# Performance work log

Hardware: AMD Instinct MI355X
Metric: run time of the kernel (lower is better)

## Reference

```python
import jax, jax.numpy as jnp
import numpy as np

K = 9          # kernel_size
PAD = K // 2   # same padding
SIGMA = 1.0
EPS = 1e-5     # BatchNorm eps


def setup_inputs() -> dict:
    key = jax.random.key(0)
    k0, k1, k2 = jax.random.split(key, 3)
    B, Cin, Cout, L = 4, 64, 64, 131072
    x = jax.random.normal(k0, (B, Cin, L), jnp.float32)
    coords = jax.random.uniform(k1, (B, 3, L), jnp.float32)  # 3D point coords in [0,1)
    W = jax.random.normal(k2, (Cout, Cin, K), jnp.float32) * (1.0 / np.sqrt(Cin * K))
    bias = jnp.zeros((Cout,), jnp.float32)
    gamma = jnp.ones((Cout,), jnp.float32)
    beta = jnp.zeros((Cout,), jnp.float32)
    return {"x": x, "coords": coords, "W": W, "bias": bias, "gamma": gamma, "beta": beta}


def reference(x, coords, W, bias, gamma, beta):
    B, Cin, L = x.shape
    # zero-pad sequence dim for 'same' conv
    xpad = jnp.pad(x, ((0, 0), (0, 0), (PAD, PAD)))
    cpad = jnp.pad(coords, ((0, 0), (0, 0), (PAD, PAD)))
    # unfold: neighbor windows of size K (K is a small compile-time constant)
    x_unf = jnp.stack([xpad[:, :, k:k + L] for k in range(K)], axis=2)   # [B,Cin,K,L]
    c_unf = jnp.stack([cpad[:, :, k:k + L] for k in range(K)], axis=2)   # [B,3,K,L]
    # Gaussian spatial weights from coord distances (WeightedConv1D)
    dist2 = jnp.sum((c_unf - coords[:, :, None, :]) ** 2, axis=1)        # [B,K,L]
    w = jnp.exp(-dist2 / (2.0 * SIGMA * SIGMA))                          # [B,K,L]
    # weighted conv: contract over (Cin, K)
    out = jnp.einsum('ock,bckl->bol', W, x_unf * w[:, None, :, :])       # [B,Cout,L]
    out = out + bias[None, :, None]
    # BatchNorm1d (training-mode batch statistics over B and L) + ReLU
    mean = out.mean(axis=(0, 2), keepdims=True)
    var = out.var(axis=(0, 2), keepdims=True)
    out = (out - mean) * jax.lax.rsqrt(var + EPS)
    out = out * gamma[None, :, None] + beta[None, :, None]
    return jax.nn.relu(out)
```

## Files before the change

kernel.cpp:

```cpp
#include <hip/hip_runtime.h>
#include <hip/hip_bf16.h>

#define KK 9
#define PADK 4
#define CIN 64
#define COUT 64
#define LSEQ 131072
#define NB 4
#define TILEL 128
#define XROWS 136
#define XRS 72
#define NTILES 1024
#define NPART 64

typedef __attribute__((ext_vector_type(8))) short v8s;
typedef __attribute__((ext_vector_type(4))) float v4f;

__device__ __forceinline__ unsigned short f2bf(float f) {
  __hip_bfloat16 h = __float2bfloat16(f);
  return *reinterpret_cast<unsigned short*>(&h);
}
__device__ __forceinline__ float bf2f(unsigned short s) {
  return __uint_as_float(((unsigned)s) << 16);
}

__device__ __forceinline__ void store_o(float* p, float v) { *p = v; }
__device__ __forceinline__ void store_o(__hip_bfloat16* p, float v) { *p = __float2bfloat16(v); }

template <int CTRL>
__device__ __forceinline__ float dppadd(float v) {
  int s = __builtin_amdgcn_update_dpp(0, __float_as_int(v), CTRL, 0xF, 0xF, true);
  return v + __int_as_float(s);
}
__device__ __forceinline__ float red16(float v) {
  v = dppadd<0xB1>(v);
  v = dppadd<0x4E>(v);
  v = dppadd<0x141>(v);
  v = dppadd<0x140>(v);
  return v;
}

__global__ void wtrans_kernel(const float* __restrict__ W, v8s* __restrict__ Wt) {
  int t = blockIdx.x * 256 + threadIdx.x;
  if (t >= KK * 2 * 4 * 64) return;
  int lane = t & 63;
  int frag = t >> 6;
  int mblk = frag & 3;
  int s    = (frag >> 2) & 1;
  int k    = frag >> 3;
  int m = lane & 15, q = lane >> 4;
  int o = mblk * 16 + m;
  union { v8s v; unsigned short h[8]; } u;
#pragma unroll
  for (int j = 0; j < 8; ++j) {
    int c = 32 * s + q * 8 + j;
    u.h[j] = f2bf(W[(o * CIN + c) * KK + k]);
  }
  Wt[t] = u.v;
}

template <typename OutT>
__global__ __launch_bounds__(256, 5)
void conv_kernel(const float* __restrict__ x, const float* __restrict__ coords,
                 const v8s* __restrict__ Wt, OutT* __restrict__ cv,
                 float* __restrict__ stat_sum, float* __restrict__ stat_sq) {
  __shared__ __align__(16) __hip_bfloat16 xt[XROWS][XRS];
  __shared__ float wt[KK][TILEL];

  const int tid  = threadIdx.x;
  const int wv   = tid >> 6;
  const int wo   = wv & 1;
  const int wl   = wv >> 1;
  const int lane = tid & 63;
  const int gw   = blockIdx.x;
  const int b    = gw >> 10;
  const int tile = gw & (NTILES - 1);
  const int l0   = tile * TILEL;
  const float* xb = x + (b * CIN) * LSEQ;
  const float* cb = coords + (b * 3) * LSEQ;
  const int m = lane & 15;
  const int q = lane >> 4;

  {
    int cg = tid & 7;
    int lc = tid >> 3;
    int c8 = cg * 8;
    float4 f[8];
#pragma unroll
    for (int t = 0; t < 8; ++t)
      f[t] = *(const float4*)(xb + (c8 + t) * LSEQ + l0 + 4 * lc);
    const float* fp = (const float*)&f[0];
#pragma unroll
    for (int j = 0; j < 4; ++j) {
      union { v8s v; unsigned short h[8]; } u;
#pragma unroll
      for (int t = 0; t < 8; ++t) u.h[t] = f2bf(fp[4 * t + j]);
      *(v8s*)&xt[4 + 4 * lc + j][c8] = u.v;
    }
  }
  if (tid < 128) {
    int side = tid >> 6;
    int c = tid & 63;
    if (side == 0) {
      float el[4] = {0.f, 0.f, 0.f, 0.f};
      if (tile != 0) {
#pragma unroll
        for (int j = 0; j < 4; ++j) el[j] = xb[c * LSEQ + l0 - 4 + j];
      }
#pragma unroll
      for (int j = 0; j < 4; ++j) xt[j][c] = __float2bfloat16(el[j]);
    } else {
      float er[4] = {0.f, 0.f, 0.f, 0.f};
      if (tile != NTILES - 1) {
#pragma unroll
        for (int j = 0; j < 4; ++j) er[j] = xb[c * LSEQ + l0 + TILEL + j];
      }
#pragma unroll
      for (int j = 0; j < 4; ++j) xt[128 + 4 + j][c] = __float2bfloat16(er[j]);
    }
  }
  if (tid < TILEL) {
    int n = tid;
    float sx = cb[l0 + n];
    float sy = cb[LSEQ + l0 + n];
    float sz = cb[2 * LSEQ + l0 + n];
#pragma unroll
    for (int k = 0; k < KK; ++k) {
      int l = l0 + n + k - PADK;
      float cx = 0.f, cy = 0.f, cz = 0.f;
      if ((unsigned)l < (unsigned)LSEQ) {
        cx = cb[l]; cy = cb[LSEQ + l]; cz = cb[2 * LSEQ + l];
      }
      float dx = cx - sx, dy = cy - sy, dz = cz - sz;
      wt[k][n] = __expf(-0.5f * (dx * dx + dy * dy + dz * dz));
    }
  }
  __syncthreads();

  v4f tot[2][4];
#pragma unroll
  for (int i = 0; i < 2; ++i)
#pragma unroll
    for (int j = 0; j < 4; ++j)
      tot[i][j] = (v4f){0.f, 0.f, 0.f, 0.f};

  const v4f z4 = (v4f){0.f, 0.f, 0.f, 0.f};
  const v8s* wp = Wt + (wo * 2) * 64 + lane;

#pragma unroll 1
  for (int k = 0; k < KK; ++k) {
    v8s a00 = wp[k * 512];
    v8s a10 = wp[k * 512 + 64];
    v8s a01 = wp[k * 512 + 256];
    v8s a11 = wp[k * 512 + 256 + 64];
#pragma unroll
    for (int nbq = 0; nbq < 4; ++nbq) {
      const __hip_bfloat16* xr = &xt[wl * 64 + nbq * 16 + m + k][0];
      v8s bf0 = *(const v8s*)(xr + q * 8);
      v8s bf1 = *(const v8s*)(xr + q * 8 + 32);
      float wk = wt[k][wl * 64 + nbq * 16 + m];
      v4f y0 = __builtin_amdgcn_mfma_f32_16x16x32_bf16(a00, bf0, z4, 0, 0, 0);
      y0     = __builtin_amdgcn_mfma_f32_16x16x32_bf16(a01, bf1, y0, 0, 0, 0);
      v4f y1 = __builtin_amdgcn_mfma_f32_16x16x32_bf16(a10, bf0, z4, 0, 0, 0);
      y1     = __builtin_amdgcn_mfma_f32_16x16x32_bf16(a11, bf1, y1, 0, 0, 0);
#pragma unroll
      for (int r = 0; r < 4; ++r) {
        tot[0][nbq][r] = __builtin_fmaf(wk, y0[r], tot[0][nbq][r]);
        tot[1][nbq][r] = __builtin_fmaf(wk, y1[r], tot[1][nbq][r]);
      }
    }
  }

  const int part = gw & (NPART - 1);
  OutT* outb = cv + (size_t)(b * COUT) * LSEQ;
#pragma unroll
  for (int mb = 0; mb < 2; ++mb) {
#pragma unroll
    for (int r = 0; r < 4; ++r) {
      int o = wo * 32 + mb * 16 + q * 4 + r;
      float s1 = 0.f, s2 = 0.f;
#pragma unroll
      for (int nbq = 0; nbq < 4; ++nbq) {
        float v = tot[mb][nbq][r];
        s1 += v;
        s2 += v * v;
        store_o(&outb[o * LSEQ + l0 + wl * 64 + nbq * 16 + m], v);
      }
      s1 = red16(s1);
      s2 = red16(s2);
      if (m == 0) {
        atomicAdd(&stat_sum[part * COUT + o], s1);
        atomicAdd(&stat_sq [part * COUT + o], s2);
      }
    }
  }
}

__global__ __launch_bounds__(256)
void finalize_kernel(const float* __restrict__ stat_sum,
                     const float* __restrict__ stat_sq,
                     const float* __restrict__ gamma,
                     const float* __restrict__ beta,
                     float* __restrict__ ss) {
  __shared__ float red[2][4][COUT];
  const int o = threadIdx.x & 63, pq = threadIdx.x >> 6;
  float s1 = 0.f, s2 = 0.f;
#pragma unroll 4
  for (int p = pq * 16; p < pq * 16 + 16; ++p) {
    s1 += stat_sum[p * COUT + o];
    s2 += stat_sq [p * COUT + o];
  }
  red[0][pq][o] = s1;
  red[1][pq][o] = s2;
  __syncthreads();
  if (threadIdx.x < 64) {
    float t1 = red[0][0][o] + red[0][1][o] + red[0][2][o] + red[0][3][o];
    float t2 = red[1][0][o] + red[1][1][o] + red[1][2][o] + red[1][3][o];
    const float invN = 1.0f / (float)(NB * LSEQ);
    float mean = t1 * invN;
    float var  = t2 * invN - mean * mean;
    float sc = gamma[o] * rsqrtf(var + 1e-5f);
    ss[o]        = sc;
    ss[COUT + o] = beta[o] - mean * sc;
  }
}

__global__ __launch_bounds__(256)
void scale_f32_kernel(float* __restrict__ data, const float* __restrict__ ss) {
  const int blk = blockIdx.x;
  const int ch = (blk >> 6) & 63;
  const float sc = ss[ch];
  const float sh = ss[COUT + ch];
  const int base = blk * 2048 + threadIdx.x * 8;
  float4 a = *(float4*)(data + base);
  float4 b = *(float4*)(data + base + 4);
  a.x = fmaxf(fmaf(a.x, sc, sh), 0.f);
  a.y = fmaxf(fmaf(a.y, sc, sh), 0.f);
  a.z = fmaxf(fmaf(a.z, sc, sh), 0.f);
  a.w = fmaxf(fmaf(a.w, sc, sh), 0.f);
  b.x = fmaxf(fmaf(b.x, sc, sh), 0.f);
  b.y = fmaxf(fmaf(b.y, sc, sh), 0.f);
  b.z = fmaxf(fmaf(b.z, sc, sh), 0.f);
  b.w = fmaxf(fmaf(b.w, sc, sh), 0.f);
  *(float4*)(data + base)     = a;
  *(float4*)(data + base + 4) = b;
}

__global__ __launch_bounds__(256)
void scale_bf16_kernel(const __hip_bfloat16* __restrict__ cvin,
                       const float* __restrict__ ss, float* __restrict__ out) {
  const int blk = blockIdx.x;
  const int ch = (blk >> 6) & 63;
  const float sc = ss[ch];
  const float sh = ss[COUT + ch];
  const int base = blk * 2048 + threadIdx.x * 8;
  union { v8s v; unsigned short h[8]; } u;
  u.v = *(const v8s*)(cvin + base);
  float r[8];
#pragma unroll
  for (int i = 0; i < 8; ++i)
    r[i] = fmaxf(fmaf(bf2f(u.h[i]), sc, sh), 0.f);
  *(float4*)(out + base)     = make_float4(r[0], r[1], r[2], r[3]);
  *(float4*)(out + base + 4) = make_float4(r[4], r[5], r[6], r[7]);
}

extern "C" void kernel_launch(void* const* d_in, const int* in_sizes, int n_in,
                              void* d_out, int out_size, void* d_ws, size_t ws_size,
                              hipStream_t stream) {
  const float* x      = (const float*)d_in[0];
  const float* coords = (const float*)d_in[1];
  const float* W      = (const float*)d_in[2];
  const float* gamma  = (const float*)d_in[4];
  const float* beta   = (const float*)d_in[5];
  float* out = (float*)d_out;
  char* ws = (char*)d_ws;

  float* stat_sum = (float*)(ws);
  float* stat_sq  = (float*)(ws + 16384);
  float* ss       = (float*)(ws + 32768);
  v8s*   Wt       = (v8s*)(ws + 40960);
  __hip_bfloat16* scratch = (__hip_bfloat16*)(ws + 131072);

  const size_t need_bf16 = (size_t)131072 + (size_t)NB * COUT * LSEQ * 2;
  const bool bf16_path = ws_size >= need_bf16;

  hipMemsetAsync(ws, 0, 32768, stream);
  wtrans_kernel<<<18, 256, 0, stream>>>(W, Wt);

  if (bf16_path) {
    conv_kernel<__hip_bfloat16><<<NB * NTILES, 256, 0, stream>>>(
        x, coords, Wt, scratch, stat_sum, stat_sq);
    finalize_kernel<<<1, 256, 0, stream>>>(stat_sum, stat_sq, gamma, beta, ss);
    scale_bf16_kernel<<<(NB * COUT * (LSEQ / 2048)), 256, 0, stream>>>(scratch, ss, out);
  } else {
    conv_kernel<float><<<NB * NTILES, 256, 0, stream>>>(
        x, coords, Wt, out, stat_sum, stat_sq);
    finalize_kernel<<<1, 256, 0, stream>>>(stat_sum, stat_sq, gamma, beta, ss);
    scale_f32_kernel<<<(NB * COUT * (LSEQ / 2048)), 256, 0, stream>>>(out, ss);
  }
}
```

Measured before the change: 320.5 us.

## Process two tiles per block with register prefetch of next tile

Each conv block now handles two consecutive sequence tiles, halving the grid. While the MFMA loop runs on the current tile, the x, halo and coord values for the next tile are loaded into registers. The Gaussian weight computation is split across all 256 threads instead of 128. This aims to hide global load latency behind compute, at the cost of more registers (possibly lower occupancy under launch_bounds 5) and fewer blocks to spread across the GPU.

```diff
diff --git a/kernel.cpp b/kernel.cpp
--- a/kernel.cpp
+++ b/kernel.cpp
@@ -12,6 +12,8 @@
 #define XRS 72
 #define NTILES 1024
 #define NPART 64
+#define TPB 2
+#define GRIDC (NB * NTILES / TPB)
 
 typedef __attribute__((ext_vector_type(8))) short v8s;
 typedef __attribute__((ext_vector_type(4))) float v4f;
@@ -72,125 +74,147 @@
   const int wo   = wv & 1;
   const int wl   = wv >> 1;
   const int lane = tid & 63;
-  const int gw   = blockIdx.x;
-  const int b    = gw >> 10;
-  const int tile = gw & (NTILES - 1);
-  const int l0   = tile * TILEL;
+  const int m = lane & 15;
+  const int q = lane >> 4;
+
+  const int bid = blockIdx.x;
+  const int b   = bid >> 9;
+  const int t0  = (bid & 511) * TPB;
   const float* xb = x + (b * CIN) * LSEQ;
   const float* cb = coords + (b * 3) * LSEQ;
-  const int m = lane & 15;
-  const int q = lane >> 4;
-
-  {
-    int cg = tid & 7;
-    int lc = tid >> 3;
-    int c8 = cg * 8;
-    float4 f[8];
+  OutT* outb = cv + (size_t)(b * COUT) * LSEQ;
+
+  const int cg8 = tid & 7, lc = tid >> 3, c8 = cg8 * 8;
+  const int cn = tid & 127, kh = tid >> 7, k0 = kh * 4;
+  const int nk = kh ? 5 : 4;
+
+  float4 f[8];
+  float4 hx;
+  float sx, sy, sz;
+  float nx[5], ny[5], nz[5];
+
+  auto prefetch = [&](int tile) {
+    const int l0 = tile * TILEL;
 #pragma unroll
     for (int t = 0; t < 8; ++t)
       f[t] = *(const float4*)(xb + (c8 + t) * LSEQ + l0 + 4 * lc);
-    const float* fp = (const float*)&f[0];
-#pragma unroll
-    for (int j = 0; j < 4; ++j) {
-      union { v8s v; unsigned short h[8]; } u;
-#pragma unroll
-      for (int t = 0; t < 8; ++t) u.h[t] = f2bf(fp[4 * t + j]);
-      *(v8s*)&xt[4 + 4 * lc + j][c8] = u.v;
-    }
-  }
-  if (tid < 128) {
-    int side = tid >> 6;
-    int c = tid & 63;
-    if (side == 0) {
-      float el[4] = {0.f, 0.f, 0.f, 0.f};
-      if (tile != 0) {
-#pragma unroll
-        for (int j = 0; j < 4; ++j) el[j] = xb[c * LSEQ + l0 - 4 + j];
-      }
-#pragma unroll
-      for (int j = 0; j < 4; ++j) xt[j][c] = __float2bfloat16(el[j]);
-    } else {
-      float er[4] = {0.f, 0.f, 0.f, 0.f};
-      if (tile != NTILES - 1) {
-#pragma unroll
-        for (int j = 0; j < 4; ++j) er[j] = xb[c * LSEQ + l0 + TILEL + j];
-      }
-#pragma unroll
-      for (int j = 0; j < 4; ++j) xt[128 + 4 + j][c] = __float2bfloat16(er[j]);
-    }
-  }
-  if (tid < TILEL) {
-    int n = tid;
-    float sx = cb[l0 + n];
-    float sy = cb[LSEQ + l0 + n];
-    float sz = cb[2 * LSEQ + l0 + n];
-#pragma unroll
+    if (tid < 128) {
+      int side = tid >> 6, c = tid & 63;
+      hx = make_float4(0.f, 0.f, 0.f, 0.f);
+      if (side == 0) {
+        if (tile != 0) hx = *(const float4*)(xb + c * LSEQ + l0 - 4);
+      } else {
+        if (tile != NTILES - 1) hx = *(const float4*)(xb + c * LSEQ + l0 + TILEL);
+      }
+    }
+    sx = cb[l0 + cn];
+    sy = cb[LSEQ + l0 + cn];
+    sz = cb[2 * LSEQ + l0 + cn];
+#pragma unroll
+    for (int i = 0; i < 5; ++i) {
+      int l = l0 + cn + (k0 + i) - PADK;
+      float cx = 0.f, cy = 0.f, cz = 0.f;
+      if (i < nk && (unsigned)l < (unsigned)LSEQ) {
+        cx = cb[l]; cy = cb[LSEQ + l]; cz = cb[2 * LSEQ + l];
+      }
+      nx[i] = cx; ny[i] = cy; nz[i] = cz;
+    }
+  };
+
+  prefetch(t0);
+
+#pragma unroll 1
+  for (int ti = 0; ti < TPB; ++ti) {
+    const int tile = t0 + ti;
+    const int l0 = tile * TILEL;
+
+    {
+      const float* fp = (const float*)&f[0];
+#pragma unroll
+      for (int j = 0; j < 4; ++j) {
+        union { v8s v; unsigned short h[8]; } u;
+#pragma unroll
+        for (int t = 0; t < 8; ++t) u.h[t] = f2bf(fp[4 * t + j]);
+        *(v8s*)&xt[4 + 4 * lc + j][c8] = u.v;
+      }
+      if (tid < 128) {
+        int side = tid >> 6, c = tid & 63;
+        int rb = side ? (TILEL + PADK) : 0;
+        xt[rb + 0][c] = __float2bfloat16(hx.x);
+        xt[rb + 1][c] = __float2bfloat16(hx.y);
+        xt[rb + 2][c] = __float2bfloat16(hx.z);
+        xt[rb + 3][c] = __float2bfloat16(hx.w);
+      }
+#pragma unroll
+      for (int i = 0; i < 5; ++i) {
+        if (i < nk) {
+          float dx = nx[i] - sx, dy = ny[i] - sy, dz = nz[i] - sz;
+          wt[k0 + i][cn] = __expf(-0.5f * (dx * dx + dy * dy + dz * dz));
+        }
+      }
+    }
+
+    if (ti + 1 < TPB) prefetch(tile + 1);
+
+    asm volatile("s_waitcnt lgkmcnt(0)" ::: "memory");
+    __builtin_amdgcn_s_barrier();
+
+    v4f tot[2][4];
+#pragma unroll
+    for (int i = 0; i < 2; ++i)
+#pragma unroll
+      for (int j = 0; j < 4; ++j)
+        tot[i][j] = (v4f){0.f, 0.f, 0.f, 0.f};
+
+    const v4f z4 = (v4f){0.f, 0.f, 0.f, 0.f};
+    const v8s* wp = Wt + (wo * 2) * 64 + lane;
+
+#pragma unroll 1
     for (int k = 0; k < KK; ++k) {
-      int l = l0 + n + k - PADK;
-      float cx = 0.f, cy = 0.f, cz = 0.f;
-      if ((unsigned)l < (unsigned)LSEQ) {
-        cx = cb[l]; cy = cb[LSEQ + l]; cz = cb[2 * LSEQ + l];
-      }
-      float dx = cx - sx, dy = cy - sy, dz = cz - sz;
-      wt[k][n] = __expf(-0.5f * (dx * dx + dy * dy + dz * dz));
-    }
-  }
-  __syncthreads();
-
-  v4f tot[2][4];
-#pragma unroll
-  for (int i = 0; i < 2; ++i)
-#pragma unroll
-    for (int j = 0; j < 4; ++j)
-      tot[i][j] = (v4f){0.f, 0.f, 0.f, 0.f};
-
-  const v4f z4 = (v4f){0.f, 0.f, 0.f, 0.f};
-  const v8s* wp = Wt + (wo * 2) * 64 + lane;
-
-#pragma unroll 1
-  for (int k = 0; k < KK; ++k) {
-    v8s a00 = wp[k * 512];
-    v8s a10 = wp[k * 512 + 64];
-    v8s a01 = wp[k * 512 + 256];
-    v8s a11 = wp[k * 512 + 256 + 64];
-#pragma unroll
-    for (int nbq = 0; nbq < 4; ++nbq) {
-      const __hip_bfloat16* xr = &xt[wl * 64 + nbq * 16 + m + k][0];
-      v8s bf0 = *(const v8s*)(xr + q * 8);
-      v8s bf1 = *(const v8s*)(xr + q * 8 + 32);
-      float wk = wt[k][wl * 64 + nbq * 16 + m];
-      v4f y0 = __builtin_amdgcn_mfma_f32_16x16x32_bf16(a00, bf0, z4, 0, 0, 0);
-      y0     = __builtin_amdgcn_mfma_f32_16x16x32_bf16(a01, bf1, y0, 0, 0, 0);
-      v4f y1 = __builtin_amdgcn_mfma_f32_16x16x32_bf16(a10, bf0, z4, 0, 0, 0);
-      y1     = __builtin_amdgcn_mfma_f32_16x16x32_bf16(a11, bf1, y1, 0, 0, 0);
+      v8s a00 = wp[k * 512];
+      v8s a10 = wp[k * 512 + 64];
+      v8s a01 = wp[k * 512 + 256];
+      v8s a11 = wp[k * 512 + 256 + 64];
+#pragma unroll
+      for (int nbq = 0; nbq < 4; ++nbq) {
+        const __hip_bfloat16* xr = &xt[wl * 64 + nbq * 16 + m + k][0];
+        v8s bf0 = *(const v8s*)(xr + q * 8);
+        v8s bf1 = *(const v8s*)(xr + q * 8 + 32);
+        float wk = wt[k][wl * 64 + nbq * 16 + m];
+        v4f y0 = __builtin_amdgcn_mfma_f32_16x16x32_bf16(a00, bf0, z4, 0, 0, 0);
+        y0     = __builtin_amdgcn_mfma_f32_16x16x32_bf16(a01, bf1, y0, 0, 0, 0);
+        v4f y1 = __builtin_amdgcn_mfma_f32_16x16x32_bf16(a10, bf0, z4, 0, 0, 0);
+        y1     = __builtin_amdgcn_mfma_f32_16x16x32_bf16(a11, bf1, y1, 0, 0, 0);
+#pragma unroll
+        for (int r = 0; r < 4; ++r) {
+          tot[0][nbq][r] = __builtin_fmaf(wk, y0[r], tot[0][nbq][r]);
+          tot[1][nbq][r] = __builtin_fmaf(wk, y1[r], tot[1][nbq][r]);
+        }
+      }
+    }
+
+    __builtin_amdgcn_s_barrier();
+
+    const int part = tile & (NPART - 1);
+#pragma unroll
+    for (int mb = 0; mb < 2; ++mb) {
 #pragma unroll
       for (int r = 0; r < 4; ++r) {
-        tot[0][nbq][r] = __builtin_fmaf(wk, y0[r], tot[0][nbq][r]);
-        tot[1][nbq][r] = __builtin_fmaf(wk, y1[r], tot[1][nbq][r]);
-      }
-    }
-  }
-
-  const int part = gw & (NPART - 1);
-  OutT* outb = cv + (size_t)(b * COUT) * LSEQ;
-#pragma unroll
-  for (int mb = 0; mb < 2; ++mb) {
-#pragma unroll
-    for (int r = 0; r < 4; ++r) {
-      int o = wo * 32 + mb * 16 + q * 4 + r;
-      float s1 = 0.f, s2 = 0.f;
-#pragma unroll
-      for (int nbq = 0; nbq < 4; ++nbq) {
-        float v = tot[mb][nbq][r];
-        s1 += v;
-        s2 += v * v;
-        store_o(&outb[o * LSEQ + l0 + wl * 64 + nbq * 16 + m], v);
-      }
-      s1 = red16(s1);
-      s2 = red16(s2);
-      if (m == 0) {
-        atomicAdd(&stat_sum[part * COUT + o], s1);
-        atomicAdd(&stat_sq [part * COUT + o], s2);
+        int o = wo * 32 + mb * 16 + q * 4 + r;
+        float s1 = 0.f, s2 = 0.f;
+#pragma unroll
+        for (int nbq = 0; nbq < 4; ++nbq) {
+          float v = tot[mb][nbq][r];
+          s1 += v;
+          s2 += v * v;
+          store_o(&outb[o * LSEQ + l0 + wl * 64 + nbq * 16 + m], v);
+        }
+        s1 = red16(s1);
+        s2 = red16(s2);
+        if (m == 0) {
+          atomicAdd(&stat_sum[part * COUT + o], s1);
+          atomicAdd(&stat_sq [part * COUT + o], s2);
+        }
       }
     }
   }
@@ -288,12 +312,12 @@
   wtrans_kernel<<<18, 256, 0, stream>>>(W, Wt);
 
   if (bf16_path) {
-    conv_kernel<__hip_bfloat16><<<NB * NTILES, 256, 0, stream>>>(
+    conv_kernel<__hip_bfloat16><<<GRIDC, 256, 0, stream>>>(
         x, coords, Wt, scratch, stat_sum, stat_sq);
     finalize_kernel<<<1, 256, 0, stream>>>(stat_sum, stat_sq, gamma, beta, ss);
     scale_bf16_kernel<<<(NB * COUT * (LSEQ / 2048)), 256, 0, stream>>>(scratch, ss, out);
   } else {
-    conv_kernel<float><<<NB * NTILES, 256, 0, stream>>>(
+    conv_kernel<float><<<GRIDC, 256, 0, stream>>>(
         x, coords, Wt, out, stat_sum, stat_sq);
     finalize_kernel<<<1, 256, 0, stream>>>(stat_sum, stat_sq, gamma, beta, ss);
     scale_f32_kernel<<<(NB * COUT * (LSEQ / 2048)), 256, 0, stream>>>(out, ss);
```

Result: slower. 418.5 us (+30.6%).

## Pre-transpose x to padded bf16 image and double-buffer conv tiles via async LDS loads

Applied to the files above, without the earlier changes.

Adds a pre-pass kernel that converts x to a padded, row-major bf16 image in workspace. The conv kernel then processes four tiles per block and stages the next tile into a second LDS buffer with global_load_lds while it computes the current one, overlapping loads with MFMA work. It also prefetches neighbour coordinates and computes the Gaussian weights for the next tile during the epilogue. In exchange it adds an extra full pass over x (read fp32, write bf16), needs more workspace and LDS per block, and keeps the old kernel as a fallback.

```diff
diff --git a/kernel.cpp b/kernel.cpp
--- a/kernel.cpp
+++ b/kernel.cpp
@@ -12,6 +12,15 @@
 #define XRS 72
 #define NTILES 1024
 #define NPART 64
+#define TPB2 4
+#define GRID2 (NB * NTILES / TPB2)
+#define IMGROWB 144
+#define IMGB 18875520ULL
+#define SLABB 18432
+#define SLABSZ 19584
+
+#define AS1 __attribute__((address_space(1)))
+#define AS3 __attribute__((address_space(3)))
 
 typedef __attribute__((ext_vector_type(8))) short v8s;
 typedef __attribute__((ext_vector_type(4))) float v4f;
@@ -26,6 +35,11 @@
 
 __device__ __forceinline__ void store_o(float* p, float v) { *p = v; }
 __device__ __forceinline__ void store_o(__hip_bfloat16* p, float v) { *p = __float2bfloat16(v); }
+
+__device__ __forceinline__ void gl_lds16(const void* g, void* l) {
+  __builtin_amdgcn_global_load_lds((const AS1 unsigned int*)g,
+                                   (AS3 unsigned int*)l, 16, 0, 0);
+}
 
 template <int CTRL>
 __device__ __forceinline__ float dppadd(float v) {
@@ -59,11 +73,184 @@
   Wt[t] = u.v;
 }
 
+__global__ __launch_bounds__(256)
+void xtrans_kernel(const float* __restrict__ x, char* __restrict__ xg) {
+  const int blk = blockIdx.x;
+  const int b = blk >> 10;
+  const int t = blk & (NTILES - 1);
+  const int l0 = t * TILEL;
+  const int tid = threadIdx.x;
+  const float* xb = x + (size_t)(b * CIN) * LSEQ;
+  char* xgb = xg + (size_t)b * IMGB;
+
+  const int cg = tid & 7, lc = tid >> 3, c8 = cg * 8;
+  float4 f[8];
+#pragma unroll
+  for (int tt = 0; tt < 8; ++tt)
+    f[tt] = *(const float4*)(xb + (c8 + tt) * LSEQ + l0 + 4 * lc);
+  const float* fp = (const float*)&f[0];
+#pragma unroll
+  for (int j = 0; j < 4; ++j) {
+    union { v8s v; unsigned short h[8]; } u;
+#pragma unroll
+    for (int tt = 0; tt < 8; ++tt) u.h[tt] = f2bf(fp[4 * tt + j]);
+    *(v8s*)(xgb + (size_t)(l0 + 4 * lc + j + 4) * IMGROWB + c8 * 2) = u.v;
+  }
+  if (t == 0 && tid < 36)
+    *(float4*)(xgb + tid * 16) = make_float4(0.f, 0.f, 0.f, 0.f);
+  if (t == NTILES - 1 && tid < 36)
+    *(float4*)(xgb + (size_t)131076 * IMGROWB + tid * 16) = make_float4(0.f, 0.f, 0.f, 0.f);
+}
+
 template <typename OutT>
 __global__ __launch_bounds__(256, 5)
-void conv_kernel(const float* __restrict__ x, const float* __restrict__ coords,
-                 const v8s* __restrict__ Wt, OutT* __restrict__ cv,
-                 float* __restrict__ stat_sum, float* __restrict__ stat_sq) {
+void conv_async(const char* __restrict__ xg, const float* __restrict__ coords,
+                const v8s* __restrict__ Wt, OutT* __restrict__ cv,
+                float* __restrict__ stat_sum, float* __restrict__ stat_sq) {
+  __shared__ __align__(16) __hip_bfloat16 xt[2][XROWS][XRS];
+  __shared__ float wt[2][KK][TILEL];
+
+  const int tid  = threadIdx.x;
+  const int wv   = tid >> 6;
+  const int wo   = wv & 1;
+  const int wl   = wv >> 1;
+  const int lane = tid & 63;
+  const int m = lane & 15;
+  const int q = lane >> 4;
+
+  const int bid = blockIdx.x;
+  const int b   = bid >> 8;
+  const int t0  = (bid & 255) * TPB2;
+  const char* xgb = xg + (size_t)b * IMGB;
+  const float* cb = coords + (size_t)(b * 3) * LSEQ;
+  OutT* outb = cv + (size_t)(b * COUT) * LSEQ;
+
+  const int cn = tid & 127, kh = tid >> 7, k0 = kh * 4;
+  const int nk = kh ? 5 : 4;
+
+  float sx, sy, sz;
+  float nx[5], ny[5], nz[5];
+
+  auto coord_issue = [&](int tile) {
+    const int l0 = tile * TILEL;
+    sx = cb[l0 + cn];
+    sy = cb[LSEQ + l0 + cn];
+    sz = cb[2 * LSEQ + l0 + cn];
+#pragma unroll
+    for (int i = 0; i < 5; ++i) {
+      int l = l0 + cn + (k0 + i) - PADK;
+      float cx = 0.f, cy = 0.f, cz = 0.f;
+      if (i < nk && (unsigned)l < (unsigned)LSEQ) {
+        cx = cb[l]; cy = cb[LSEQ + l]; cz = cb[2 * LSEQ + l];
+      }
+      nx[i] = cx; ny[i] = cy; nz[i] = cz;
+    }
+  };
+
+  auto stage = [&](int tile, int nxt) {
+    const char* src = xgb + (size_t)tile * SLABB + wv * 4896;
+    char* dst = (char*)&xt[nxt][0][0] + wv * 4896;
+#pragma unroll
+    for (int j = 0; j < 4; ++j)
+      gl_lds16(src + j * 1024 + lane * 16, dst + j * 1024);
+    if (lane < 50)
+      gl_lds16(src + 4096 + lane * 16, dst + 4096);
+  };
+
+  auto wt_write = [&](int nxt) {
+#pragma unroll
+    for (int i = 0; i < 5; ++i) {
+      if (i < nk) {
+        float dx = nx[i] - sx, dy = ny[i] - sy, dz = nz[i] - sz;
+        wt[nxt][k0 + i][cn] = __expf(-0.5f * (dx * dx + dy * dy + dz * dz));
+      }
+    }
+  };
+
+  coord_issue(t0);
+  stage(t0, 0);
+  wt_write(0);
+  __syncthreads();
+
+#pragma unroll 1
+  for (int ti = 0; ti < TPB2; ++ti) {
+    const int tile = t0 + ti;
+    const int l0 = tile * TILEL;
+    const int cur = ti & 1;
+
+    v4f tot[2][4];
+#pragma unroll
+    for (int i = 0; i < 2; ++i)
+#pragma unroll
+      for (int j = 0; j < 4; ++j)
+        tot[i][j] = (v4f){0.f, 0.f, 0.f, 0.f};
+
+    const v4f z4 = (v4f){0.f, 0.f, 0.f, 0.f};
+    const v8s* wp = Wt + (wo * 2) * 64 + lane;
+
+#pragma unroll 1
+    for (int k = 0; k < KK; ++k) {
+      v8s a00 = wp[k * 512];
+      v8s a10 = wp[k * 512 + 64];
+      v8s a01 = wp[k * 512 + 256];
+      v8s a11 = wp[k * 512 + 320];
+#pragma unroll
+      for (int nbq = 0; nbq < 4; ++nbq) {
+        const __hip_bfloat16* xr = &xt[cur][wl * 64 + nbq * 16 + m + k][0];
+        v8s bf0 = *(const v8s*)(xr + q * 8);
+        v8s bf1 = *(const v8s*)(xr + q * 8 + 32);
+        float wk = wt[cur][k][wl * 64 + nbq * 16 + m];
+        v4f y0 = __builtin_amdgcn_mfma_f32_16x16x32_bf16(a00, bf0, z4, 0, 0, 0);
+        y0     = __builtin_amdgcn_mfma_f32_16x16x32_bf16(a01, bf1, y0, 0, 0, 0);
+        v4f y1 = __builtin_amdgcn_mfma_f32_16x16x32_bf16(a10, bf0, z4, 0, 0, 0);
+        y1     = __builtin_amdgcn_mfma_f32_16x16x32_bf16(a11, bf1, y1, 0, 0, 0);
+#pragma unroll
+        for (int r = 0; r < 4; ++r) {
+          tot[0][nbq][r] = __builtin_fmaf(wk, y0[r], tot[0][nbq][r]);
+          tot[1][nbq][r] = __builtin_fmaf(wk, y1[r], tot[1][nbq][r]);
+        }
+      }
+    }
+
+    if (ti + 1 < TPB2) {
+      coord_issue(tile + 1);
+      stage(tile + 1, cur ^ 1);
+    }
+
+    const int part = tile & (NPART - 1);
+#pragma unroll
+    for (int mb = 0; mb < 2; ++mb) {
+#pragma unroll
+      for (int r = 0; r < 4; ++r) {
+        int o = wo * 32 + mb * 16 + q * 4 + r;
+        float s1 = 0.f, s2 = 0.f;
+#pragma unroll
+        for (int nbq = 0; nbq < 4; ++nbq) {
+          float v = tot[mb][nbq][r];
+          s1 += v;
+          s2 += v * v;
+          store_o(&outb[o * LSEQ + l0 + wl * 64 + nbq * 16 + m], v);
+        }
+        s1 = red16(s1);
+        s2 = red16(s2);
+        if (m == 0) {
+          atomicAdd(&stat_sum[part * COUT + o], s1);
+          atomicAdd(&stat_sq [part * COUT + o], s2);
+        }
+      }
+    }
+
+    if (ti + 1 < TPB2) wt_write(cur ^ 1);
+
+    __syncthreads();
+  }
+}
+
+template <typename OutT>
+__global__ __launch_bounds__(256, 5)
+void conv_fallback(const float* __restrict__ x, const float* __restrict__ coords,
+                   const v8s* __restrict__ Wt, OutT* __restrict__ cv,
+                   float* __restrict__ stat_sum, float* __restrict__ stat_sq) {
   __shared__ __align__(16) __hip_bfloat16 xt[XROWS][XRS];
   __shared__ float wt[KK][TILEL];
 
@@ -76,8 +263,8 @@
   const int b    = gw >> 10;
   const int tile = gw & (NTILES - 1);
   const int l0   = tile * TILEL;
-  const float* xb = x + (b * CIN) * LSEQ;
-  const float* cb = coords + (b * 3) * LSEQ;
+  const float* xb = x + (size_t)(b * CIN) * LSEQ;
+  const float* cb = coords + (size_t)(b * 3) * LSEQ;
   const int m = lane & 15;
   const int q = lane >> 4;
 
@@ -152,7 +339,7 @@
     v8s a00 = wp[k * 512];
     v8s a10 = wp[k * 512 + 64];
     v8s a01 = wp[k * 512 + 256];
-    v8s a11 = wp[k * 512 + 256 + 64];
+    v8s a11 = wp[k * 512 + 320];
 #pragma unroll
     for (int nbq = 0; nbq < 4; ++nbq) {
       const __hip_bfloat16* xr = &xt[wl * 64 + nbq * 16 + m + k][0];
@@ -279,21 +466,39 @@
   float* stat_sq  = (float*)(ws + 16384);
   float* ss       = (float*)(ws + 32768);
   v8s*   Wt       = (v8s*)(ws + 40960);
-  __hip_bfloat16* scratch = (__hip_bfloat16*)(ws + 131072);
-
-  const size_t need_bf16 = (size_t)131072 + (size_t)NB * COUT * LSEQ * 2;
-  const bool bf16_path = ws_size >= need_bf16;
+
+  char*  xg       = ws + 131072;
+  const size_t xg_end    = 131072ULL + 4ULL * IMGB;
+  const size_t scr_bytes = (size_t)NB * COUT * LSEQ * 2;
+
+  const size_t need_full = xg_end + scr_bytes;
+  const size_t need_xg   = xg_end;
+  const size_t need_old  = 131072ULL + scr_bytes;
 
   hipMemsetAsync(ws, 0, 32768, stream);
   wtrans_kernel<<<18, 256, 0, stream>>>(W, Wt);
 
-  if (bf16_path) {
-    conv_kernel<__hip_bfloat16><<<NB * NTILES, 256, 0, stream>>>(
+  if (ws_size >= need_full) {
+    __hip_bfloat16* scratch = (__hip_bfloat16*)(ws + xg_end);
+    xtrans_kernel<<<NB * NTILES, 256, 0, stream>>>(x, xg);
+    conv_async<__hip_bfloat16><<<GRID2, 256, 0, stream>>>(
+        xg, coords, Wt, scratch, stat_sum, stat_sq);
+    finalize_kernel<<<1, 256, 0, stream>>>(stat_sum, stat_sq, gamma, beta, ss);
+    scale_bf16_kernel<<<(NB * COUT * (LSEQ / 2048)), 256, 0, stream>>>(scratch, ss, out);
+  } else if (ws_size >= need_xg) {
+    xtrans_kernel<<<NB * NTILES, 256, 0, stream>>>(x, xg);
+    conv_async<float><<<GRID2, 256, 0, stream>>>(
+        xg, coords, Wt, out, stat_sum, stat_sq);
+    finalize_kernel<<<1, 256, 0, stream>>>(stat_sum, stat_sq, gamma, beta, ss);
+    scale_f32_kernel<<<(NB * COUT * (LSEQ / 2048)), 256, 0, stream>>>(out, ss);
+  } else if (ws_size >= need_old) {
+    __hip_bfloat16* scratch = (__hip_bfloat16*)(ws + 131072);
+    conv_fallback<__hip_bfloat16><<<NB * NTILES, 256, 0, stream>>>(
         x, coords, Wt, scratch, stat_sum, stat_sq);
     finalize_kernel<<<1, 256, 0, stream>>>(stat_sum, stat_sq, gamma, beta, ss);
     scale_bf16_kernel<<<(NB * COUT * (LSEQ / 2048)), 256, 0, stream>>>(scratch, ss, out);
   } else {
-    conv_kernel<float><<<NB * NTILES, 256, 0, stream>>>(
+    conv_fallback<float><<<NB * NTILES, 256, 0, stream>>>(
         x, coords, Wt, out, stat_sum, stat_sq);
     finalize_kernel<<<1, 256, 0, stream>>>(stat_sum, stat_sq, gamma, beta, ss);
     scale_f32_kernel<<<(NB * COUT * (LSEQ / 2048)), 256, 0, stream>>>(out, ss);
```

New measurement: 377.1 us. 17.7% more time.
